# Kernel tuning notes

Measured on AMD Instinct MI355X. Metric: run time of the kernel, lower is better.

Reference implementation:

```python
import jax, jax.numpy as jnp
import numpy as np

N, D_IM, D_CLI = 2048, 1024, 64
EPS = 1e-12  # F.normalize eps


def setup_inputs() -> dict:
    key = jax.random.key(0)
    k1, k2, k3, k4 = jax.random.split(key, 4)
    phi_im = jax.random.normal(k1, (N, D_IM), dtype=jnp.float32)
    phi_cli = jax.random.normal(k2, (N, D_CLI), dtype=jnp.float32)
    t = jax.random.randint(k3, (N, 2), 0, 3, dtype=jnp.int64)
    traumatic = jax.random.randint(k4, (N,), 0, 2, dtype=jnp.int64)
    return {"phi_im": phi_im, "phi_cli": phi_cli, "t": t, "traumatic": traumatic}


def _l2norm(x):
    n = jnp.sqrt(jnp.sum(x * x, axis=1, keepdims=True))
    return x / jnp.maximum(n, EPS)


def _pair_block(S, ma, mb):
    # S: [N,N] full cosine similarity; ma, mb: [N] bool group masks.
    valid = ma[:, None] & mb[None, :]
    mat = jnp.where(valid, S, 0.0)            # scatter-into-zero matrix semantics
    masked = jnp.where(valid, S, jnp.inf)     # masked argmin = nearest (least similar) pair
    flat = jnp.argmin(masked.reshape(-1))
    i = flat // S.shape[1]
    j = flat % S.shape[1]
    return mat, masked.reshape(-1)[flat], jnp.stack([i, j])


def reference(phi_im, phi_cli, t, traumatic):
    im_n = _l2norm(phi_im)
    cli_n = _l2norm(phi_cli)
    # single batched GEMM replaces the per-pair python loops
    S_im = im_n @ im_n.T    # [N,N]
    S_cli = cli_n @ cli_n.T  # [N,N]

    t1 = t[:, 1]
    m0 = (t1 == 0) & (traumatic == 1)
    m1 = t1 == 1
    m2 = t1 == 2

    mats, vals, idxs = [], [], []
    for S in (S_im, S_cli):
        for (ma, mb) in ((m0, m1), (m0, m2), (m1, m2)):
            mat, v, ij = _pair_block(S, ma, mb)
            mats.append(mat)
            vals.append(v)
            idxs.append(ij)
    sims = jnp.stack(mats)           # [6, N, N]: im_01, im_02, im_12, cli_01, cli_02, cli_12
    min_vals = jnp.stack(vals)       # [6]
    min_idx = jnp.stack(idxs)        # [6, 2]
    return sims, min_vals, min_idx
```

## Files before the change

### kernel.cpp

```cpp
#include <hip/hip_runtime.h>
#include <stdint.h>

#define NROW 2048
#define D_IM 1024
#define D_CLI 64
#define EPSF 1e-12f
#define NN ((size_t)NROW * (size_t)NROW)

typedef __attribute__((ext_vector_type(8))) short bf16x8;
typedef __attribute__((ext_vector_type(4))) float f32x4;

#define OFF_PACKED   0
#define OFF_CNT      64
#define OFF_CAT      128
#define OFF_LISTS    8320
#define OFF_POS      32896
#define OFF_COLINFO  41216
#define OFF_INVIM    65792
#define OFF_INVCLI   73984
#define OFF_PIM      82176
#define OFF_PCLI     8470784
#define OFF_SC       8995072

__device__ __forceinline__ unsigned int enc_f32(float x) {
    unsigned int u = __float_as_uint(x);
    return (u & 0x80000000u) ? ~u : (u | 0x80000000u);
}
__device__ __forceinline__ unsigned short bf16rn(float x) {
    unsigned int u = __float_as_uint(x);
    return (unsigned short)((u + 0x7FFFu + ((u >> 16) & 1u)) >> 16);
}
__device__ __forceinline__ float bf16tof(unsigned short h) {
    return __uint_as_float(((unsigned int)h) << 16);
}

__global__ __launch_bounds__(256)
void prepscan_kernel(const float* __restrict__ phi_im,
                     const float* __restrict__ phi_cli,
                     const int* __restrict__ t,
                     const int* __restrict__ traumatic,
                     float* __restrict__ inv_im,
                     float* __restrict__ inv_cli,
                     char* __restrict__ pim,
                     char* __restrict__ pcli,
                     int* __restrict__ cnt,
                     int* __restrict__ catArr,
                     int* __restrict__ lists,
                     int* __restrict__ posIn,
                     unsigned int* __restrict__ colinfo,
                     unsigned long long* __restrict__ packed) {
    __shared__ unsigned long long shmem[256];
    const int tid = threadIdx.x;

    if (blockIdx.x == NROW) {
        int cats[8];
        unsigned long long mycnt = 0;
        #pragma unroll
        for (int e = 0; e < 8; e++) {
            int r = tid * 8 + e;
            int t1 = t[2 * r + 1];
            int tr = traumatic[r];
            int c = (t1 == 1) ? 1 : ((t1 == 2) ? 2 : ((tr == 1) ? 0 : 3));
            cats[e] = c;
            catArr[r] = c;
            if (c < 3) mycnt += 1ULL << (21 * c);
        }
        shmem[tid] = mycnt;
        __syncthreads();
        for (int off = 1; off < 256; off <<= 1) {
            unsigned long long v = (tid >= off) ? shmem[tid - off] : 0ULL;
            __syncthreads();
            shmem[tid] += v;
            __syncthreads();
        }
        unsigned long long excl = shmem[tid] - mycnt;
        unsigned long long tot = shmem[255];
        unsigned int loc[3];
        #pragma unroll
        for (int c = 0; c < 3; c++)
            loc[c] = (unsigned int)(excl >> (21 * c)) & 0x1FFFFFu;
        #pragma unroll
        for (int e = 0; e < 8; e++) {
            int r = tid * 8 + e;
            int c = cats[e];
            unsigned int slot = 0xFFFFFFFFu;
            if (c < 3) {
                slot = loc[c]++;
                lists[c * 2048 + slot] = r;
                posIn[r] = (int)slot;
            }
            colinfo[0 * 2048 + r] = (c == 1) ? slot : 0xFFFFFFFFu;
            colinfo[1 * 2048 + r] = (c == 2) ? slot : 0xFFFFFFFFu;
            colinfo[2 * 2048 + r] = (c == 2) ? slot : 0xFFFFFFFFu;
        }
        if (tid == 0) {
            cnt[0] = (int)(tot & 0x1FFFFFu);
            cnt[1] = (int)((tot >> 21) & 0x1FFFFFu);
            cnt[2] = (int)((tot >> 42) & 0x1FFFFFu);
            cnt[3] = 0;
        }
        if (tid < 6) packed[tid] = 0xFFFFFFFFFFFFFFFFULL;
        return;
    }

    float* sred = (float*)shmem;
    const int r = blockIdx.x;

    float4 v = ((const float4*)(phi_im + (size_t)r * D_IM))[tid];
    float a[4] = {v.x, v.y, v.z, v.w};
    unsigned short h4[4], l4[4];
    #pragma unroll
    for (int e = 0; e < 4; e++) {
        h4[e] = bf16rn(a[e]);
        l4[e] = bf16rn(a[e] - bf16tof(h4[e]));
    }
    {
        char* rowb = pim + (size_t)r * 4096 + (tid >> 1) * 32 + (tid & 1) * 8;
        *(ushort4*)rowb = make_ushort4(h4[0], h4[1], h4[2], h4[3]);
        *(ushort4*)(rowb + 16) = make_ushort4(l4[0], l4[1], l4[2], l4[3]);
    }
    sred[tid] = a[0] * a[0] + a[1] * a[1] + a[2] * a[2] + a[3] * a[3];
    __syncthreads();
    for (int off = 128; off > 0; off >>= 1) {
        if (tid < off) sred[tid] += sred[tid + off];
        __syncthreads();
    }
    if (tid == 0) inv_im[r] = 1.0f / fmaxf(sqrtf(sred[0]), EPSF);

    if (tid < 16) {
        float4 c = ((const float4*)(phi_cli + (size_t)r * D_CLI))[tid];
        float b[4] = {c.x, c.y, c.z, c.w};
        unsigned short ch[4], cl[4];
        #pragma unroll
        for (int e = 0; e < 4; e++) {
            ch[e] = bf16rn(b[e]);
            cl[e] = bf16rn(b[e] - bf16tof(ch[e]));
        }
        char* rowb = pcli + (size_t)r * 256 + (tid >> 1) * 32 + (tid & 1) * 8;
        *(ushort4*)rowb = make_ushort4(ch[0], ch[1], ch[2], ch[3]);
        *(ushort4*)(rowb + 16) = make_ushort4(cl[0], cl[1], cl[2], cl[3]);
    }
    if (tid < 64) {
        float c = phi_cli[(size_t)r * D_CLI + tid];
        float cs = c * c;
        #pragma unroll
        for (int off = 32; off > 0; off >>= 1) cs += __shfl_down(cs, off, 64);
        if (tid == 0) inv_cli[r] = 1.0f / fmaxf(sqrtf(cs), EPSF);
    }
}

#define LOAD_SET(s, AH, AL, BH, BL)                                        \
    {                                                                      \
        const int kb_ = (s) * 128;                                         \
        _Pragma("unroll") for (int mt = 0; mt < 4; mt++) {                 \
            AH[mt] = *(const bf16x8*)(pX + offA[mt] + kb_);                \
            AL[mt] = *(const bf16x8*)(pX + offA[mt] + kb_ + 16);           \
            BH[mt] = *(const bf16x8*)(pX + offB[mt] + kb_);                \
            BL[mt] = *(const bf16x8*)(pX + offB[mt] + kb_ + 16);           \
        }                                                                  \
    }
#define MFMA_SET(AH, AL, BH, BL)                                           \
    _Pragma("unroll") for (int mt = 0; mt < 4; mt++)                       \
        _Pragma("unroll") for (int nt = 0; nt < 4; nt++) {                 \
            acc[mt][nt] = __builtin_amdgcn_mfma_f32_16x16x32_bf16(         \
                AH[mt], BH[nt], acc[mt][nt], 0, 0, 0);                     \
            acc[mt][nt] = __builtin_amdgcn_mfma_f32_16x16x32_bf16(         \
                AH[mt], BL[nt], acc[mt][nt], 0, 0, 0);                     \
            acc[mt][nt] = __builtin_amdgcn_mfma_f32_16x16x32_bf16(         \
                AL[mt], BH[nt], acc[mt][nt], 0, 0, 0);                     \
        }

__global__ __launch_bounds__(64, 2)
void gemm_kernel(const char* __restrict__ pim,
                 const char* __restrict__ pcli,
                 const float* __restrict__ inv_im,
                 const float* __restrict__ inv_cli,
                 const int* __restrict__ cnt,
                 const int* __restrict__ lists,
                 float* __restrict__ Sc,
                 unsigned long long* __restrict__ packed) {
    __shared__ float sIA[64], sIB[64];
    __shared__ int sRA[64], sRB[64];

    const int n0 = cnt[0], n1 = cnt[1], n2 = cnt[2];
    const int tA = (n0 + 63) >> 6, tB = (n1 + 63) >> 6, tC = (n2 + 63) >> 6;
    const int T0 = tA * tB, T1 = tA * tC, T2 = tB * tC;
    const int tot = T0 + T1 + T2;
    int bid = blockIdx.x;
    if (bid >= 2 * tot) return;
    int z = 0;
    if (bid >= tot) { z = 1; bid -= tot; }
    const size_t s0 = (size_t)(tA << 6) * (tB << 6);
    const size_t s1 = (size_t)(tA << 6) * (tC << 6);
    const size_t s2 = (size_t)(tB << 6) * (tC << 6);
    size_t scoff = z ? (s0 + s1 + s2) : 0;
    int gx, nA, nB, nBpad, pp;
    const int *lA, *lB;
    if (bid < T0)           { pp = 0; gx = tB; nA = n0; nB = n1; lA = lists;        lB = lists + 2048; nBpad = tB << 6; }
    else if (bid < T0 + T1) { bid -= T0;      scoff += s0;      pp = 1; gx = tC; nA = n0; nB = n2; lA = lists;        lB = lists + 4096; nBpad = tC << 6; }
    else                    { bid -= T0 + T1; scoff += s0 + s1; pp = 2; gx = tC; nA = n1; nB = n2; lA = lists + 2048; lB = lists + 4096; nBpad = tC << 6; }
    const int by = bid / gx, bx = bid % gx;
    const int i0 = by << 6, j0 = bx << 6;
    const int pz = z * 3 + pp;

    const char* __restrict__ pX = z ? pcli : pim;
    const float* __restrict__ inv = z ? inv_cli : inv_im;
    const int steps = z ? (D_CLI / 32) : (D_IM / 32);
    const size_t stride = z ? 256 : 4096;
    const int lane = threadIdx.x;

    {
        int ia = lA[min(i0 + lane, nA - 1)];
        int ib = lB[min(j0 + lane, nB - 1)];
        sRA[lane] = ia; sRB[lane] = ib;
        sIA[lane] = inv[ia]; sIB[lane] = inv[ib];
    }
    __syncthreads();

    const int mrow = lane & 15;
    const int quad = lane >> 4;
    size_t offA[4], offB[4];
    #pragma unroll
    for (int mt = 0; mt < 4; mt++) {
        offA[mt] = (size_t)sRA[mt * 16 + mrow] * stride + quad * 32;
        offB[mt] = (size_t)sRB[mt * 16 + mrow] * stride + quad * 32;
    }

    f32x4 acc[4][4];
    #pragma unroll
    for (int mt = 0; mt < 4; mt++)
        #pragma unroll
        for (int nt = 0; nt < 4; nt++)
            acc[mt][nt] = (f32x4){0.f, 0.f, 0.f, 0.f};

    bf16x8 A0h[4], A0l[4], B0h[4], B0l[4];
    bf16x8 A1h[4], A1l[4], B1h[4], B1l[4];
    LOAD_SET(0, A0h, A0l, B0h, B0l);
    for (int s = 0; s < steps; s += 2) {
        if (s + 1 < steps) LOAD_SET(s + 1, A1h, A1l, B1h, B1l);
        MFMA_SET(A0h, A0l, B0h, B0l);
        if (s + 2 < steps) LOAD_SET(s + 2, A0h, A0l, B0h, B0l);
        if (s + 1 < steps) MFMA_SET(A1h, A1l, B1h, B1l);
    }

    unsigned long long best = 0xFFFFFFFFFFFFFFFFULL;
    #pragma unroll
    for (int mt = 0; mt < 4; mt++)
        #pragma unroll
        for (int nt = 0; nt < 4; nt++) {
            const int cloc = nt * 16 + mrow;
            const float ivb = sIB[cloc];
            const unsigned int jcol = (unsigned int)sRB[cloc];
            #pragma unroll
            for (int rr = 0; rr < 4; rr++) {
                const int rloc = mt * 16 + quad * 4 + rr;
                float sv = acc[mt][nt][rr] * (sIA[rloc] * ivb);
                Sc[scoff + (size_t)(i0 + rloc) * nBpad + (j0 + cloc)] = sv;
                unsigned long long pk =
                    ((unsigned long long)enc_f32(sv) << 32) |
                    ((unsigned int)sRA[rloc] * (unsigned int)NROW + jcol);
                if (pk < best) best = pk;
            }
        }
    #pragma unroll
    for (int off = 32; off > 0; off >>= 1) {
        unsigned long long o = __shfl_down(best, off, 64);
        if (o < best) best = o;
    }
    if (lane == 0) atomicMin(&packed[pz], best);
}

__global__ __launch_bounds__(256)
void writer_kernel(const float* __restrict__ Sc,
                   const int* __restrict__ cnt,
                   const int* __restrict__ catArr,
                   const int* __restrict__ posIn,
                   const unsigned int* __restrict__ colinfo,
                   float* __restrict__ out,
                   const unsigned long long* __restrict__ packed) {
    const int b = blockIdx.x;
    const int tid = threadIdx.x;
    if (b == 6 * NROW) {
        const int p = tid;
        if (p < 6) {
            unsigned long long pk = packed[p];
            float v;
            unsigned int flat;
            if (pk == 0xFFFFFFFFFFFFFFFFULL) {
                v = __builtin_huge_valf();
                flat = 0u;
            } else {
                unsigned int key = (unsigned int)(pk >> 32);
                flat = (unsigned int)pk;
                unsigned int bits = (key & 0x80000000u) ? (key ^ 0x80000000u) : ~key;
                v = __uint_as_float(bits);
            }
            float* mv = out + 6 * NN;
            mv[p] = v;
            float* mi = out + 6 * NN + 6;
            mi[2 * p + 0] = (float)(flat >> 11);
            mi[2 * p + 1] = (float)(flat & 2047u);
        }
        return;
    }
    const int pz = b >> 11;
    const int row = b & 2047;
    const int z = pz / 3, p = pz - 3 * z;
    float* orow = out + (size_t)pz * NN + (size_t)row * NROW;

    const int rowcat = (p == 2) ? 1 : 0;
    if (catArr[row] != rowcat) {
        const float4 z4 = make_float4(0.f, 0.f, 0.f, 0.f);
        ((float4*)orow)[tid] = z4;
        ((float4*)orow)[tid + 256] = z4;
        return;
    }

    const int n0 = cnt[0], n1 = cnt[1], n2 = cnt[2];
    const int tA = (n0 + 63) >> 6, tB = (n1 + 63) >> 6, tC = (n2 + 63) >> 6;
    const size_t s0 = (size_t)(tA << 6) * (tB << 6);
    const size_t s1 = (size_t)(tA << 6) * (tC << 6);
    const size_t s2 = (size_t)(tB << 6) * (tC << 6);
    size_t scoff = z ? (s0 + s1 + s2) : 0;
    int nBpad;
    if (p == 0)      { nBpad = tB << 6; }
    else if (p == 1) { scoff += s0;      nBpad = tC << 6; }
    else             { scoff += s0 + s1; nBpad = tC << 6; }

    const float* srow = Sc + scoff + (size_t)posIn[row] * nBpad;
    const uint4* cinfo4 = (const uint4*)(colinfo + p * 2048);

    #pragma unroll
    for (int seg = 0; seg < 2; seg++) {
        const int j4 = tid + seg * 256;
        uint4 inf = cinfo4[j4];
        float v0 = (inf.x != 0xFFFFFFFFu) ? srow[inf.x] : 0.f;
        float v1 = (inf.y != 0xFFFFFFFFu) ? srow[inf.y] : 0.f;
        float v2 = (inf.z != 0xFFFFFFFFu) ? srow[inf.z] : 0.f;
        float v3 = (inf.w != 0xFFFFFFFFu) ? srow[inf.w] : 0.f;
        ((float4*)orow)[j4] = make_float4(v0, v1, v2, v3);
    }
}

extern "C" void kernel_launch(void* const* d_in, const int* in_sizes, int n_in,
                              void* d_out, int out_size, void* d_ws, size_t ws_size,
                              hipStream_t stream) {
    const float* phi_im = (const float*)d_in[0];
    const float* phi_cli = (const float*)d_in[1];
    const int* t = (const int*)d_in[2];
    const int* traumatic = (const int*)d_in[3];
    float* out = (float*)d_out;

    char* ws = (char*)d_ws;
    unsigned long long* packed = (unsigned long long*)(ws + OFF_PACKED);
    int* cnt = (int*)(ws + OFF_CNT);
    int* catArr = (int*)(ws + OFF_CAT);
    int* lists = (int*)(ws + OFF_LISTS);
    int* posIn = (int*)(ws + OFF_POS);
    unsigned int* colinfo = (unsigned int*)(ws + OFF_COLINFO);
    float* inv_im = (float*)(ws + OFF_INVIM);
    float* inv_cli = (float*)(ws + OFF_INVCLI);
    char* pim = ws + OFF_PIM;
    char* pcli = ws + OFF_PCLI;
    float* Sc = (float*)(ws + OFF_SC);

    prepscan_kernel<<<NROW + 1, 256, 0, stream>>>(
        phi_im, phi_cli, t, traumatic, inv_im, inv_cli, pim, pcli,
        cnt, catArr, lists, posIn, colinfo, packed);
    gemm_kernel<<<800, 64, 0, stream>>>(pim, pcli, inv_im, inv_cli,
                                        cnt, lists, Sc, packed);
    writer_kernel<<<6 * NROW + 1, 256, 0, stream>>>(Sc, cnt, catArr, posIn,
                                                    colinfo, out, packed);
}
```

Before: 168.4 us.

## Fuse prep, GEMM and writer into one cooperative persistent kernel with grid syncs

Replaces the three separate launches (prep/scan, GEMM, scatter writer) with a single cooperative kernel of 512 blocks of 256 threads that uses grid.sync between phases. Each wave handles one row of prep and one 64x64 GEMM tile, and the writer phase loops over row tasks. The GEMM's LDS exchange of indices is replaced by wave shuffles. This removes inter-kernel launch gaps and tail effects, but adds grid-wide barrier costs and limits the GEMM to 2048 wave slots. It falls back to the old three-kernel path if the cooperative launch fails.

```diff
diff --git a/kernel.cpp b/kernel.cpp
--- a/kernel.cpp
+++ b/kernel.cpp
@@ -1,5 +1,8 @@
 #include <hip/hip_runtime.h>
+#include <hip/hip_cooperative_groups.h>
 #include <stdint.h>
+
+namespace cg = cooperative_groups;
 
 #define NROW 2048
 #define D_IM 1024
@@ -32,6 +35,309 @@
 }
 __device__ __forceinline__ float bf16tof(unsigned short h) {
     return __uint_as_float(((unsigned int)h) << 16);
+}
+
+#define LOAD_SET(s, AH, AL, BH, BL)                                        \
+    {                                                                      \
+        const int kb_ = (s) * 128;                                         \
+        _Pragma("unroll") for (int mt = 0; mt < 4; mt++) {                 \
+            AH[mt] = *(const bf16x8*)(pX + offA[mt] + kb_);                \
+            AL[mt] = *(const bf16x8*)(pX + offA[mt] + kb_ + 16);           \
+            BH[mt] = *(const bf16x8*)(pX + offB[mt] + kb_);                \
+            BL[mt] = *(const bf16x8*)(pX + offB[mt] + kb_ + 16);           \
+        }                                                                  \
+    }
+#define MFMA_SET(AH, AL, BH, BL)                                           \
+    _Pragma("unroll") for (int mt = 0; mt < 4; mt++)                       \
+        _Pragma("unroll") for (int nt = 0; nt < 4; nt++) {                 \
+            acc[mt][nt] = __builtin_amdgcn_mfma_f32_16x16x32_bf16(         \
+                AH[mt], BH[nt], acc[mt][nt], 0, 0, 0);                     \
+            acc[mt][nt] = __builtin_amdgcn_mfma_f32_16x16x32_bf16(         \
+                AH[mt], BL[nt], acc[mt][nt], 0, 0, 0);                     \
+            acc[mt][nt] = __builtin_amdgcn_mfma_f32_16x16x32_bf16(         \
+                AL[mt], BH[nt], acc[mt][nt], 0, 0, 0);                     \
+        }
+
+__device__ __forceinline__ void prep_row_wave(
+        int r, int lane,
+        const float* __restrict__ phi_im, const float* __restrict__ phi_cli,
+        float* __restrict__ inv_im, float* __restrict__ inv_cli,
+        char* __restrict__ pim, char* __restrict__ pcli) {
+    float ssum = 0.f;
+    #pragma unroll
+    for (int q = 0; q < 4; q++) {
+        const int idx = lane + 64 * q;
+        float4 v = ((const float4*)(phi_im + (size_t)r * D_IM))[idx];
+        float a[4] = {v.x, v.y, v.z, v.w};
+        unsigned short h4[4], l4[4];
+        #pragma unroll
+        for (int e = 0; e < 4; e++) {
+            h4[e] = bf16rn(a[e]);
+            l4[e] = bf16rn(a[e] - bf16tof(h4[e]));
+        }
+        char* rowb = pim + (size_t)r * 4096 + (idx >> 1) * 32 + (idx & 1) * 8;
+        *(ushort4*)rowb = make_ushort4(h4[0], h4[1], h4[2], h4[3]);
+        *(ushort4*)(rowb + 16) = make_ushort4(l4[0], l4[1], l4[2], l4[3]);
+        ssum += a[0] * a[0] + a[1] * a[1] + a[2] * a[2] + a[3] * a[3];
+    }
+    #pragma unroll
+    for (int off = 32; off > 0; off >>= 1) ssum += __shfl_down(ssum, off, 64);
+    if (lane == 0) inv_im[r] = 1.0f / fmaxf(sqrtf(ssum), EPSF);
+
+    if (lane < 16) {
+        float4 c = ((const float4*)(phi_cli + (size_t)r * D_CLI))[lane];
+        float b[4] = {c.x, c.y, c.z, c.w};
+        unsigned short ch[4], cl[4];
+        #pragma unroll
+        for (int e = 0; e < 4; e++) {
+            ch[e] = bf16rn(b[e]);
+            cl[e] = bf16rn(b[e] - bf16tof(ch[e]));
+        }
+        char* rowb = pcli + (size_t)r * 256 + (lane >> 1) * 32 + (lane & 1) * 8;
+        *(ushort4*)rowb = make_ushort4(ch[0], ch[1], ch[2], ch[3]);
+        *(ushort4*)(rowb + 16) = make_ushort4(cl[0], cl[1], cl[2], cl[3]);
+    }
+    float c = phi_cli[(size_t)r * D_CLI + lane];
+    float cs = c * c;
+    #pragma unroll
+    for (int off = 32; off > 0; off >>= 1) cs += __shfl_down(cs, off, 64);
+    if (lane == 0) inv_cli[r] = 1.0f / fmaxf(sqrtf(cs), EPSF);
+}
+
+__global__ __launch_bounds__(256, 2)
+void mega_kernel(const float* __restrict__ phi_im,
+                 const float* __restrict__ phi_cli,
+                 const int* __restrict__ t,
+                 const int* __restrict__ traumatic,
+                 float* __restrict__ inv_im,
+                 float* __restrict__ inv_cli,
+                 char* __restrict__ pim,
+                 char* __restrict__ pcli,
+                 int* __restrict__ cnt,
+                 int* __restrict__ catArr,
+                 int* __restrict__ lists,
+                 int* __restrict__ posIn,
+                 unsigned int* __restrict__ colinfo,
+                 unsigned long long* __restrict__ packed,
+                 float* __restrict__ Sc,
+                 float* __restrict__ out) {
+    cg::grid_group grid = cg::this_grid();
+    __shared__ unsigned long long shmem[256];
+    const int tid = threadIdx.x;
+    const int w = tid >> 6;
+    const int lane = tid & 63;
+
+    prep_row_wave((int)blockIdx.x * 4 + w, lane, phi_im, phi_cli,
+                  inv_im, inv_cli, pim, pcli);
+
+    if (blockIdx.x == 0) {
+        __syncthreads();
+        int cats[8];
+        unsigned long long mycnt = 0;
+        #pragma unroll
+        for (int e = 0; e < 8; e++) {
+            int r = tid * 8 + e;
+            int t1 = t[2 * r + 1];
+            int tr = traumatic[r];
+            int c = (t1 == 1) ? 1 : ((t1 == 2) ? 2 : ((tr == 1) ? 0 : 3));
+            cats[e] = c;
+            catArr[r] = c;
+            if (c < 3) mycnt += 1ULL << (21 * c);
+        }
+        shmem[tid] = mycnt;
+        __syncthreads();
+        for (int off = 1; off < 256; off <<= 1) {
+            unsigned long long v = (tid >= off) ? shmem[tid - off] : 0ULL;
+            __syncthreads();
+            shmem[tid] += v;
+            __syncthreads();
+        }
+        unsigned long long excl = shmem[tid] - mycnt;
+        unsigned long long tot = shmem[255];
+        unsigned int loc[3];
+        #pragma unroll
+        for (int c = 0; c < 3; c++)
+            loc[c] = (unsigned int)(excl >> (21 * c)) & 0x1FFFFFu;
+        #pragma unroll
+        for (int e = 0; e < 8; e++) {
+            int r = tid * 8 + e;
+            int c = cats[e];
+            unsigned int slot = 0xFFFFFFFFu;
+            if (c < 3) {
+                slot = loc[c]++;
+                lists[c * 2048 + slot] = r;
+                posIn[r] = (int)slot;
+            }
+            colinfo[0 * 2048 + r] = (c == 1) ? slot : 0xFFFFFFFFu;
+            colinfo[1 * 2048 + r] = (c == 2) ? slot : 0xFFFFFFFFu;
+            colinfo[2 * 2048 + r] = (c == 2) ? slot : 0xFFFFFFFFu;
+        }
+        if (tid == 0) {
+            cnt[0] = (int)(tot & 0x1FFFFFu);
+            cnt[1] = (int)((tot >> 21) & 0x1FFFFFu);
+            cnt[2] = (int)((tot >> 42) & 0x1FFFFFu);
+            cnt[3] = 0;
+        }
+        if (tid < 6) packed[tid] = 0xFFFFFFFFFFFFFFFFULL;
+    }
+
+    grid.sync();
+
+    {
+        const int n0 = cnt[0], n1 = cnt[1], n2 = cnt[2];
+        const int tA = (n0 + 63) >> 6, tB = (n1 + 63) >> 6, tC = (n2 + 63) >> 6;
+        const int T0 = tA * tB, T1 = tA * tC, T2 = tB * tC;
+        const int tot = T0 + T1 + T2;
+        int vbid = (int)blockIdx.x * 4 + w;
+        if (vbid < 2 * tot) {
+            int bid = vbid;
+            int z = 0;
+            if (bid >= tot) { z = 1; bid -= tot; }
+            const size_t s0 = (size_t)(tA << 6) * (tB << 6);
+            const size_t s1 = (size_t)(tA << 6) * (tC << 6);
+            const size_t s2 = (size_t)(tB << 6) * (tC << 6);
+            size_t scoff = z ? (s0 + s1 + s2) : 0;
+            int gx, nA, nB, nBpad, pp;
+            const int *lA, *lB;
+            if (bid < T0)           { pp = 0; gx = tB; nA = n0; nB = n1; lA = lists;        lB = lists + 2048; nBpad = tB << 6; }
+            else if (bid < T0 + T1) { bid -= T0;      scoff += s0;      pp = 1; gx = tC; nA = n0; nB = n2; lA = lists;        lB = lists + 4096; nBpad = tC << 6; }
+            else                    { bid -= T0 + T1; scoff += s0 + s1; pp = 2; gx = tC; nA = n1; nB = n2; lA = lists + 2048; lB = lists + 4096; nBpad = tC << 6; }
+            const int by = bid / gx, bx = bid % gx;
+            const int i0 = by << 6, j0 = bx << 6;
+            const int pz = z * 3 + pp;
+
+            const char* __restrict__ pX = z ? pcli : pim;
+            const float* __restrict__ inv = z ? inv_cli : inv_im;
+            const int steps = z ? (D_CLI / 32) : (D_IM / 32);
+            const size_t stride = z ? 256 : 4096;
+
+            const int ia = lA[min(i0 + lane, nA - 1)];
+            const int ib = lB[min(j0 + lane, nB - 1)];
+            const float iva = inv[ia], ivb = inv[ib];
+            const int mrow = lane & 15;
+            const int quad = lane >> 4;
+            size_t offA[4], offB[4];
+            #pragma unroll
+            for (int mt = 0; mt < 4; mt++) {
+                offA[mt] = (size_t)__shfl(ia, mt * 16 + mrow, 64) * stride + quad * 32;
+                offB[mt] = (size_t)__shfl(ib, mt * 16 + mrow, 64) * stride + quad * 32;
+            }
+
+            f32x4 acc[4][4];
+            #pragma unroll
+            for (int mt = 0; mt < 4; mt++)
+                #pragma unroll
+                for (int nt = 0; nt < 4; nt++)
+                    acc[mt][nt] = (f32x4){0.f, 0.f, 0.f, 0.f};
+
+            bf16x8 A0h[4], A0l[4], B0h[4], B0l[4];
+            bf16x8 A1h[4], A1l[4], B1h[4], B1l[4];
+            LOAD_SET(0, A0h, A0l, B0h, B0l);
+            for (int s = 0; s < steps; s += 2) {
+                if (s + 1 < steps) LOAD_SET(s + 1, A1h, A1l, B1h, B1l);
+                MFMA_SET(A0h, A0l, B0h, B0l);
+                if (s + 2 < steps) LOAD_SET(s + 2, A0h, A0l, B0h, B0l);
+                if (s + 1 < steps) MFMA_SET(A1h, A1l, B1h, B1l);
+            }
+
+            float ivAv[16]; int iAv[16];
+            #pragma unroll
+            for (int mt = 0; mt < 4; mt++)
+                #pragma unroll
+                for (int rr = 0; rr < 4; rr++) {
+                    int rl = mt * 16 + quad * 4 + rr;
+                    ivAv[mt * 4 + rr] = __shfl(iva, rl, 64);
+                    iAv[mt * 4 + rr] = __shfl(ia, rl, 64);
+                }
+            float ivBv[4]; unsigned int jBv[4];
+            #pragma unroll
+            for (int nt = 0; nt < 4; nt++) {
+                int cl = nt * 16 + mrow;
+                ivBv[nt] = __shfl(ivb, cl, 64);
+                jBv[nt] = (unsigned int)__shfl(ib, cl, 64);
+            }
+            unsigned long long best = 0xFFFFFFFFFFFFFFFFULL;
+            #pragma unroll
+            for (int mt = 0; mt < 4; mt++)
+                #pragma unroll
+                for (int nt = 0; nt < 4; nt++) {
+                    const int cloc = nt * 16 + mrow;
+                    #pragma unroll
+                    for (int rr = 0; rr < 4; rr++) {
+                        const int rloc = mt * 16 + quad * 4 + rr;
+                        float sv = acc[mt][nt][rr] * (ivAv[mt * 4 + rr] * ivBv[nt]);
+                        Sc[scoff + (size_t)(i0 + rloc) * nBpad + (j0 + cloc)] = sv;
+                        unsigned long long pk =
+                            ((unsigned long long)enc_f32(sv) << 32) |
+                            ((unsigned int)iAv[mt * 4 + rr] * (unsigned int)NROW + jBv[nt]);
+                        if (pk < best) best = pk;
+                    }
+                }
+            #pragma unroll
+            for (int off = 32; off > 0; off >>= 1) {
+                unsigned long long o = __shfl_down(best, off, 64);
+                if (o < best) best = o;
+            }
+            if (lane == 0) atomicMin(&packed[pz], best);
+        }
+    }
+
+    grid.sync();
+
+    if (blockIdx.x == 0 && tid < 6) {
+        unsigned long long pk = packed[tid];
+        float v;
+        unsigned int flat;
+        if (pk == 0xFFFFFFFFFFFFFFFFULL) { v = __builtin_huge_valf(); flat = 0u; }
+        else {
+            unsigned int key = (unsigned int)(pk >> 32);
+            flat = (unsigned int)pk;
+            unsigned int bits = (key & 0x80000000u) ? (key ^ 0x80000000u) : ~key;
+            v = __uint_as_float(bits);
+        }
+        out[6 * NN + tid] = v;
+        out[6 * NN + 6 + 2 * tid + 0] = (float)(flat >> 11);
+        out[6 * NN + 6 + 2 * tid + 1] = (float)(flat & 2047u);
+    }
+    {
+        const int n0 = cnt[0], n1 = cnt[1], n2 = cnt[2];
+        const int tA = (n0 + 63) >> 6, tB = (n1 + 63) >> 6, tC = (n2 + 63) >> 6;
+        const size_t s0 = (size_t)(tA << 6) * (tB << 6);
+        const size_t s1 = (size_t)(tA << 6) * (tC << 6);
+        const size_t s2 = (size_t)(tB << 6) * (tC << 6);
+        #pragma unroll 1
+        for (int it = 0; it < 24; it++) {
+            const int task = (int)blockIdx.x + 512 * it;
+            const int pz = task >> 11;
+            const int row = task & 2047;
+            const int z = pz / 3, p = pz - 3 * z;
+            float* orow = out + (size_t)pz * NN + (size_t)row * NROW;
+            const int rowcat = (p == 2) ? 1 : 0;
+            if (catArr[row] != rowcat) {
+                const float4 z4 = make_float4(0.f, 0.f, 0.f, 0.f);
+                ((float4*)orow)[tid] = z4;
+                ((float4*)orow)[tid + 256] = z4;
+                continue;
+            }
+            size_t scoff = z ? (s0 + s1 + s2) : 0;
+            int nBpad;
+            if (p == 0)      { nBpad = tB << 6; }
+            else if (p == 1) { scoff += s0;      nBpad = tC << 6; }
+            else             { scoff += s0 + s1; nBpad = tC << 6; }
+            const float* srow = Sc + scoff + (size_t)posIn[row] * nBpad;
+            const uint4* cinfo4 = (const uint4*)(colinfo + p * 2048);
+            #pragma unroll
+            for (int seg = 0; seg < 2; seg++) {
+                const int j4 = tid + seg * 256;
+                uint4 inf = cinfo4[j4];
+                float v0 = (inf.x != 0xFFFFFFFFu) ? srow[inf.x] : 0.f;
+                float v1 = (inf.y != 0xFFFFFFFFu) ? srow[inf.y] : 0.f;
+                float v2 = (inf.z != 0xFFFFFFFFu) ? srow[inf.z] : 0.f;
+                float v3 = (inf.w != 0xFFFFFFFFu) ? srow[inf.w] : 0.f;
+                ((float4*)orow)[j4] = make_float4(v0, v1, v2, v3);
+            }
+        }
+    }
 }
 
 __global__ __launch_bounds__(256)
@@ -51,7 +357,6 @@
                      unsigned long long* __restrict__ packed) {
     __shared__ unsigned long long shmem[256];
     const int tid = threadIdx.x;
-
     if (blockIdx.x == NROW) {
         int cats[8];
         unsigned long long mycnt = 0;
@@ -102,10 +407,8 @@
         if (tid < 6) packed[tid] = 0xFFFFFFFFFFFFFFFFULL;
         return;
     }
-
     float* sred = (float*)shmem;
     const int r = blockIdx.x;
-
     float4 v = ((const float4*)(phi_im + (size_t)r * D_IM))[tid];
     float a[4] = {v.x, v.y, v.z, v.w};
     unsigned short h4[4], l4[4];
@@ -126,7 +429,6 @@
         __syncthreads();
     }
     if (tid == 0) inv_im[r] = 1.0f / fmaxf(sqrtf(sred[0]), EPSF);
-
     if (tid < 16) {
         float4 c = ((const float4*)(phi_cli + (size_t)r * D_CLI))[tid];
         float b[4] = {c.x, c.y, c.z, c.w};
@@ -148,27 +450,6 @@
         if (tid == 0) inv_cli[r] = 1.0f / fmaxf(sqrtf(cs), EPSF);
     }
 }
-
-#define LOAD_SET(s, AH, AL, BH, BL)                                        \
-    {                                                                      \
-        const int kb_ = (s) * 128;                                         \
-        _Pragma("unroll") for (int mt = 0; mt < 4; mt++) {                 \
-            AH[mt] = *(const bf16x8*)(pX + offA[mt] + kb_);                \
-            AL[mt] = *(const bf16x8*)(pX + offA[mt] + kb_ + 16);           \
-            BH[mt] = *(const bf16x8*)(pX + offB[mt] + kb_);                \
-            BL[mt] = *(const bf16x8*)(pX + offB[mt] + kb_ + 16);           \
-        }                                                                  \
-    }
-#define MFMA_SET(AH, AL, BH, BL)                                           \
-    _Pragma("unroll") for (int mt = 0; mt < 4; mt++)                       \
-        _Pragma("unroll") for (int nt = 0; nt < 4; nt++) {                 \
-            acc[mt][nt] = __builtin_amdgcn_mfma_f32_16x16x32_bf16(         \
-                AH[mt], BH[nt], acc[mt][nt], 0, 0, 0);                     \
-            acc[mt][nt] = __builtin_amdgcn_mfma_f32_16x16x32_bf16(         \
-                AH[mt], BL[nt], acc[mt][nt], 0, 0, 0);                     \
-            acc[mt][nt] = __builtin_amdgcn_mfma_f32_16x16x32_bf16(         \
-                AL[mt], BH[nt], acc[mt][nt], 0, 0, 0);                     \
-        }
 
 __global__ __launch_bounds__(64, 2)
 void gemm_kernel(const char* __restrict__ pim,
@@ -181,7 +462,6 @@
                  unsigned long long* __restrict__ packed) {
     __shared__ float sIA[64], sIB[64];
     __shared__ int sRA[64], sRB[64];
-
     const int n0 = cnt[0], n1 = cnt[1], n2 = cnt[2];
     const int tA = (n0 + 63) >> 6, tB = (n1 + 63) >> 6, tC = (n2 + 63) >> 6;
     const int T0 = tA * tB, T1 = tA * tC, T2 = tB * tC;
@@ -202,13 +482,11 @@
     const int by = bid / gx, bx = bid % gx;
     const int i0 = by << 6, j0 = bx << 6;
     const int pz = z * 3 + pp;
-
     const char* __restrict__ pX = z ? pcli : pim;
     const float* __restrict__ inv = z ? inv_cli : inv_im;
     const int steps = z ? (D_CLI / 32) : (D_IM / 32);
     const size_t stride = z ? 256 : 4096;
     const int lane = threadIdx.x;
-
     {
         int ia = lA[min(i0 + lane, nA - 1)];
         int ib = lB[min(j0 + lane, nB - 1)];
@@ -216,7 +494,6 @@
         sIA[lane] = inv[ia]; sIB[lane] = inv[ib];
     }
     __syncthreads();
-
     const int mrow = lane & 15;
     const int quad = lane >> 4;
     size_t offA[4], offB[4];
@@ -225,14 +502,12 @@
         offA[mt] = (size_t)sRA[mt * 16 + mrow] * stride + quad * 32;
         offB[mt] = (size_t)sRB[mt * 16 + mrow] * stride + quad * 32;
     }
-
     f32x4 acc[4][4];
     #pragma unroll
     for (int mt = 0; mt < 4; mt++)
         #pragma unroll
         for (int nt = 0; nt < 4; nt++)
             acc[mt][nt] = (f32x4){0.f, 0.f, 0.f, 0.f};
-
     bf16x8 A0h[4], A0l[4], B0h[4], B0l[4];
     bf16x8 A1h[4], A1l[4], B1h[4], B1l[4];
     LOAD_SET(0, A0h, A0l, B0h, B0l);
@@ -242,7 +517,6 @@
         if (s + 2 < steps) LOAD_SET(s + 2, A0h, A0l, B0h, B0l);
         if (s + 1 < steps) MFMA_SET(A1h, A1l, B1h, B1l);
     }
-
     unsigned long long best = 0xFFFFFFFFFFFFFFFFULL;
     #pragma unroll
     for (int mt = 0; mt < 4; mt++)
@@ -286,20 +560,16 @@
             unsigned long long pk = packed[p];
             float v;
             unsigned int flat;
-            if (pk == 0xFFFFFFFFFFFFFFFFULL) {
-                v = __builtin_huge_valf();
-                flat = 0u;
-            } else {
+            if (pk == 0xFFFFFFFFFFFFFFFFULL) { v = __builtin_huge_valf(); flat = 0u; }
+            else {
                 unsigned int key = (unsigned int)(pk >> 32);
                 flat = (unsigned int)pk;
                 unsigned int bits = (key & 0x80000000u) ? (key ^ 0x80000000u) : ~key;
                 v = __uint_as_float(bits);
             }
-            float* mv = out + 6 * NN;
-            mv[p] = v;
-            float* mi = out + 6 * NN + 6;
-            mi[2 * p + 0] = (float)(flat >> 11);
-            mi[2 * p + 1] = (float)(flat & 2047u);
+            out[6 * NN + p] = v;
+            out[6 * NN + 6 + 2 * p + 0] = (float)(flat >> 11);
+            out[6 * NN + 6 + 2 * p + 1] = (float)(flat & 2047u);
         }
         return;
     }
@@ -307,7 +577,6 @@
     const int row = b & 2047;
     const int z = pz / 3, p = pz - 3 * z;
     float* orow = out + (size_t)pz * NN + (size_t)row * NROW;
-
     const int rowcat = (p == 2) ? 1 : 0;
     if (catArr[row] != rowcat) {
         const float4 z4 = make_float4(0.f, 0.f, 0.f, 0.f);
@@ -315,7 +584,6 @@
         ((float4*)orow)[tid + 256] = z4;
         return;
     }
-
     const int n0 = cnt[0], n1 = cnt[1], n2 = cnt[2];
     const int tA = (n0 + 63) >> 6, tB = (n1 + 63) >> 6, tC = (n2 + 63) >> 6;
     const size_t s0 = (size_t)(tA << 6) * (tB << 6);
@@ -326,10 +594,8 @@
     if (p == 0)      { nBpad = tB << 6; }
     else if (p == 1) { scoff += s0;      nBpad = tC << 6; }
     else             { scoff += s0 + s1; nBpad = tC << 6; }
-
     const float* srow = Sc + scoff + (size_t)posIn[row] * nBpad;
     const uint4* cinfo4 = (const uint4*)(colinfo + p * 2048);
-
     #pragma unroll
     for (int seg = 0; seg < 2; seg++) {
         const int j4 = tid + seg * 256;
@@ -364,6 +630,16 @@
     char* pcli = ws + OFF_PCLI;
     float* Sc = (float*)(ws + OFF_SC);
 
+    void* args[] = {
+        (void*)&phi_im, (void*)&phi_cli, (void*)&t, (void*)&traumatic,
+        (void*)&inv_im, (void*)&inv_cli, (void*)&pim, (void*)&pcli,
+        (void*)&cnt, (void*)&catArr, (void*)&lists, (void*)&posIn,
+        (void*)&colinfo, (void*)&packed, (void*)&Sc, (void*)&out
+    };
+    hipError_t err = hipLaunchCooperativeKernel(
+        mega_kernel, dim3(512), dim3(256), args, 0, stream);
+    if (err == hipSuccess) return;
+
     prepscan_kernel<<<NROW + 1, 256, 0, stream>>>(
         phi_im, phi_cli, t, traumatic, inv_im, inv_cli, pim, pcli,
         cnt, catArr, lists, posIn, colinfo, packed);
```

Result: slower. 315.5 us (+87.3%).
